# Kernel tuning notes

Measured on AMD Instinct MI355X. Metric: run time of the kernel, lower is better.

Reference implementation:

```python
import jax, jax.numpy as jnp
import numpy as np
from jax import lax

DIM = 128
HEADS = 4
HEAD_DIM = DIM // HEADS          # 32
SR = 2
BN_EPS = 1e-5


def setup_inputs() -> dict:
    key = jax.random.key(0)
    ks = jax.random.split(key, 16)
    B, N, C = 8, 3136, DIM
    H = W = 56
    Nkv = (H // SR) * (W // SR)  # 784
    s = 0.05
    inp = {
        "x": jax.random.normal(ks[0], (B, N, C), jnp.float32),
        "relative_pos": jax.random.normal(ks[1], (HEADS, N, Nkv), jnp.float32),
        "Wq": jax.random.normal(ks[2], (C, C), jnp.float32) * s,
        "bq": jnp.zeros((C,), jnp.float32),
        "Wk": jax.random.normal(ks[3], (C, C), jnp.float32) * s,
        "bk": jnp.zeros((C,), jnp.float32),
        "Wv": jax.random.normal(ks[4], (C, C), jnp.float32) * s,
        "bv": jnp.zeros((C,), jnp.float32),
        "conv_w": jax.random.normal(ks[5], (C, 1, SR, SR), jnp.float32) * s,  # depthwise OIHW
        "conv_b": jnp.zeros((C,), jnp.float32),
        "bn_gamma": jnp.ones((C,), jnp.float32),
        "bn_beta": jnp.zeros((C,), jnp.float32),
        "bn_mean": jax.random.normal(ks[6], (C,), jnp.float32) * 0.1,
        "bn_var": jax.random.uniform(ks[7], (C,), jnp.float32, 0.5, 1.5),
        "Wp": jax.random.normal(ks[8], (C, C), jnp.float32) * s,
        "bp": jnp.zeros((C,), jnp.float32),
        "H": H,
        "W": W,
    }
    return inp


def reference(x, relative_pos, Wq, bq, Wk, bk, Wv, bv, conv_w, conv_b,
              bn_gamma, bn_beta, bn_mean, bn_var, Wp, bp, H, W):
    B, N, C = x.shape
    scale = HEAD_DIM ** -0.5

    # q: (B, heads, N, head_dim)
    q = (x @ Wq + bq).reshape(B, N, HEADS, HEAD_DIM).transpose(0, 2, 1, 3)

    # spatial reduction: depthwise conv stride SR + BatchNorm (eval, running stats)
    x_img = x.transpose(0, 2, 1).reshape(B, C, H, W)
    y = lax.conv_general_dilated(
        x_img, conv_w, window_strides=(SR, SR), padding="VALID",
        feature_group_count=C,
        dimension_numbers=("NCHW", "OIHW", "NCHW")) + conv_b[None, :, None, None]
    inv = bn_gamma * lax.rsqrt(bn_var + BN_EPS)
    y = y * inv[None, :, None, None] + (bn_beta - bn_mean * inv)[None, :, None, None]
    x_ = y.reshape(B, C, -1).transpose(0, 2, 1)  # (B, Nkv, C)
    Nkv = x_.shape[1]

    k = (x_ @ Wk + bk).reshape(B, Nkv, HEADS, HEAD_DIM).transpose(0, 2, 1, 3)
    v = (x_ @ Wv + bv).reshape(B, Nkv, HEADS, HEAD_DIM).transpose(0, 2, 1, 3)

    attn = jnp.einsum("bhnd,bhmd->bhnm", q, k) * scale + relative_pos[None]
    attn = jax.nn.softmax(attn, axis=-1)
    out = jnp.einsum("bhnm,bhmd->bhnd", attn, v)
    out = out.transpose(0, 2, 1, 3).reshape(B, N, C)
    return out @ Wp + bp
```

## Files before the change

kernel.cpp:

```cpp
#include <hip/hip_runtime.h>
#include <hip/hip_bf16.h>

#define BATCH 8
#define NQ 3136
#define CDIM 128
#define NHEAD 4
#define HD 32
#define NKV 784
#define HIMG 56
#define SCALE 0.17677669529663687f

typedef __attribute__((ext_vector_type(8))) short bf8_t;
typedef __attribute__((ext_vector_type(4))) float f4_t;

using bf16 = __hip_bfloat16;
using u16  = unsigned short;

static __device__ __forceinline__ float b2f(bf16 v){ return __bfloat162float(v); }
static __device__ __forceinline__ bf16  f2b(float v){ return __float2bfloat16(v); }
static __device__ __forceinline__ short f2s(float v){
  union { bf16 b; short s; } u; u.b = f2b(v); return u.s;
}
static __device__ __forceinline__ float ld1(const void* p, size_t i, int f){
  return f ? b2f(((const bf16*)p)[i]) : ((const float*)p)[i];
}
static __device__ __forceinline__ bf8_t ld8(const void* p, size_t i, int f){
  if (f) return *(const bf8_t*)((const bf16*)p + i);
  const float* fp = (const float*)p + i;
  float4 a = *(const float4*)fp;
  float4 b = *(const float4*)(fp + 4);
  bf8_t r;
  r[0] = f2s(a.x); r[1] = f2s(a.y); r[2] = f2s(a.z); r[3] = f2s(a.w);
  r[4] = f2s(b.x); r[5] = f2s(b.y); r[6] = f2s(b.z); r[7] = f2s(b.w);
  return r;
}

__global__ __launch_bounds__(64) void detect_kernel(const void* var_raw, int* flag)
{
  int lane = threadIdx.x;
  const u16* h = (const u16*)var_raw;
  bool ok = true;
  #pragma unroll
  for (int t = 0; t < 2; t++){
    union { u16 u; bf16 b; } cv; cv.u = h[lane + 64 * t];
    float v = b2f(cv.b);
    ok = ok && (v > 0.3f) && (v < 1.7f);
  }
  unsigned long long ball = __ballot(ok);
  if (lane == 0) *flag = (ball == 0xFFFFFFFFFFFFFFFFull) ? 1 : 0;
}

__global__ __launch_bounds__(256) void prep_w_kernel(
    const void* __restrict__ Wq, const void* __restrict__ Wk,
    const void* __restrict__ Wv, const void* __restrict__ Wp,
    bf16* __restrict__ Wqt, bf16* __restrict__ Wkt,
    bf16* __restrict__ Wvt, bf16* __restrict__ Wpt, const int* flag)
{
  int f = *flag;
  int idx = blockIdx.x * 256 + threadIdx.x;
  int mat = idx >> 14;
  int e   = idx & 16383;
  int i = e >> 7, o = e & 127;
  const void* src; bf16* dst; float s = 1.f;
  if      (mat == 0){ src = Wq; dst = Wqt; s = SCALE; }
  else if (mat == 1){ src = Wk; dst = Wkt; }
  else if (mat == 2){ src = Wv; dst = Wvt; }
  else              { src = Wp; dst = Wpt; }
  dst[o * 128 + i] = f2b(ld1(src, e, f) * s);
}

__global__ __launch_bounds__(256) void prep_small_kernel(
    const void* bq, const void* bk, const void* bv, const void* bp,
    const void* cw, const void* cb, const void* gam, const void* bet,
    const void* mea, const void* var,
    bf16* bqs, bf16* bks, bf16* bvs, bf16* bps,
    float* cwf, float* inv, float* shift2, const int* flag)
{
  int f = *flag;
  int t = threadIdx.x;
  if (t < 128){
    bqs[t] = f2b(ld1(bq, t, f) * SCALE);
    bks[t] = f2b(ld1(bk, t, f));
    bvs[t] = f2b(ld1(bv, t, f));
    bps[t] = f2b(ld1(bp, t, f));
    float iv = ld1(gam, t, f) * rsqrtf(ld1(var, t, f) + 1e-5f);
    inv[t] = iv;
    shift2[t] = ld1(bet, t, f) - ld1(mea, t, f) * iv + ld1(cb, t, f) * iv;
  }
  cwf[t]       = ld1(cw, t, f);
  cwf[t + 256] = ld1(cw, t + 256, f);
}

__global__ __launch_bounds__(256) void reduce_kernel(
    const void* __restrict__ x, const float* __restrict__ cwf,
    const float* __restrict__ inv, const float* __restrict__ shift2,
    bf16* __restrict__ xr, const int* flag)
{
  int f = *flag;
  int idx = blockIdx.x * 256 + threadIdx.x;
  int c  = idx & 127;
  int t  = idx >> 7;
  int b  = t / NKV;
  int kv = t - b * NKV;
  int i = kv / 28, j = kv - i * 28;
  size_t base = (size_t)(b * NQ + (2 * i) * HIMG + 2 * j) * CDIM + c;
  float acc = ld1(x, base, f)                    * cwf[c * 4 + 0]
            + ld1(x, base + CDIM, f)             * cwf[c * 4 + 1]
            + ld1(x, base + HIMG * CDIM, f)      * cwf[c * 4 + 2]
            + ld1(x, base + HIMG * CDIM + CDIM, f) * cwf[c * 4 + 3];
  xr[idx] = f2b(acc * inv[c] + shift2[c]);
}

template<int MODE>
__global__ __launch_bounds__(256) void gemm_kernel(
    const bf16* A0, const bf16* A1, const bf16* __restrict__ Wt,
    const bf16* __restrict__ bias, void* outp, const int* flag)
{
  int f = *flag;
  const bf16* A = (MODE == 2) ? (f ? A0 : A1) : A0;
  int wave = threadIdx.x >> 6, lane = threadIdx.x & 63;
  int m = lane & 15, g = lane >> 4;
  int task = blockIdx.x * 4 + wave;
  int row0 = task * 16;

  const bf16* ap = A + (size_t)(row0 + m) * CDIM + 8 * g;
  bf8_t a[4];
  #pragma unroll
  for (int ks = 0; ks < 4; ks++) a[ks] = *(const bf8_t*)(ap + 32 * ks);

  f4_t acc[8];
  #pragma unroll
  for (int ct = 0; ct < 8; ct++){
    f4_t c = {0.f, 0.f, 0.f, 0.f};
    const bf16* bp = Wt + (size_t)(ct * 16 + m) * CDIM + 8 * g;
    #pragma unroll
    for (int ks = 0; ks < 4; ks++){
      bf8_t bfr = *(const bf8_t*)(bp + 32 * ks);
      c = __builtin_amdgcn_mfma_f32_16x16x32_bf16(a[ks], bfr, c, 0, 0, 0);
    }
    acc[ct] = c;
  }

  if (MODE == 0){
    bf16* out = (bf16*)outp;
    #pragma unroll
    for (int ct = 0; ct < 8; ct++){
      int col = ct * 16 + m;
      float bv = b2f(bias[col]);
      #pragma unroll
      for (int r = 0; r < 4; r++)
        out[(size_t)(row0 + 4 * g + r) * CDIM + col] = f2b(acc[ct][r] + bv);
    }
  } else if (MODE == 1){
    bf16* out = (bf16*)outp;
    int b   = row0 / NKV;
    int kv0 = row0 - b * NKV + 4 * g;
    #pragma unroll
    for (int ct = 0; ct < 8; ct++){
      int col = ct * 16 + m;
      float bv = b2f(bias[col]);
      int h = col >> 5, d = col & 31;
      union { bf16 hh[4]; uint2 u; } pk;
      #pragma unroll
      for (int r = 0; r < 4; r++) pk.hh[r] = f2b(acc[ct][r] + bv);
      *(uint2*)((bf16*)outp + (size_t)((b * NHEAD + h) * HD + d) * NKV + kv0) = pk.u;
    }
  } else {
    #pragma unroll
    for (int ct = 0; ct < 8; ct++){
      int col = ct * 16 + m;
      float bv = b2f(bias[col]);
      #pragma unroll
      for (int r = 0; r < 4; r++){
        size_t oi = (size_t)(row0 + 4 * g + r) * CDIM + col;
        float v = acc[ct][r] + bv;
        if (f) ((bf16*)outp)[oi] = f2b(v);
        else   ((float*)outp)[oi] = v;
      }
    }
  }
}

template<int T>
static __device__ __forceinline__ void attn_chunk(
    int kv0, const bf16* __restrict__ kbase,
    const bf16* __restrict__ vb0, const bf16* __restrict__ vb1,
    const void* __restrict__ rel, size_t relidx, int f, bf16* pl, int m, int g,
    bf8_t q8, float m_run[4], float l_run[4], f4_t& O0, f4_t& O1)
{
  f4_t s[T];
  #pragma unroll
  for (int t = 0; t < T; t++){
    bf8_t k8 = *(const bf8_t*)(kbase + (size_t)(kv0 + t * 16) * CDIM);
    f4_t z = {0.f, 0.f, 0.f, 0.f};
    s[t] = __builtin_amdgcn_mfma_f32_16x16x32_bf16(q8, k8, z, 0, 0, 0);
  }
  #pragma unroll
  for (int t = 0; t < T; t++){
    #pragma unroll
    for (int r = 0; r < 4; r++)
      s[t][r] += ld1(rel, relidx + (size_t)r * NKV + kv0 + t * 16, f);
  }
  float mloc[4];
  #pragma unroll
  for (int r = 0; r < 4; r++){
    float v = s[0][r];
    #pragma unroll
    for (int t = 1; t < T; t++) v = fmaxf(v, s[t][r]);
    mloc[r] = v;
  }
  #pragma unroll
  for (int xm = 1; xm < 16; xm <<= 1){
    #pragma unroll
    for (int r = 0; r < 4; r++)
      mloc[r] = fmaxf(mloc[r], __shfl_xor(mloc[r], xm, 64));
  }
  #pragma unroll
  for (int r = 0; r < 4; r++){
    float mn = fmaxf(m_run[r], mloc[r]);
    float al = __expf(m_run[r] - mn);
    m_run[r] = mn;
    l_run[r] *= al;
    O0[r] *= al; O1[r] *= al;
  }
  #pragma unroll
  for (int t = 0; t < T; t++){
    #pragma unroll
    for (int r = 0; r < 4; r++){
      float p = __expf(s[t][r] - m_run[r]);
      l_run[r] += p;
      pl[(4 * g + r) * 136 + t * 16 + m] = f2b(p);
    }
  }
  __syncthreads();
  constexpr int NKS = (T + 1) / 2;
  #pragma unroll
  for (int ks = 0; ks < NKS; ks++){
    bf8_t a8 = *(const bf8_t*)(pl + m * 136 + ks * 32 + 8 * g);
    bf8_t v0, v1;
    if (T == 1 && g >= 2){
      bf8_t z8 = {0, 0, 0, 0, 0, 0, 0, 0};
      a8 = z8; v0 = z8; v1 = z8;
    } else {
      v0 = *(const bf8_t*)(vb0 + kv0 + ks * 32 + 8 * g);
      v1 = *(const bf8_t*)(vb1 + kv0 + ks * 32 + 8 * g);
    }
    O0 = __builtin_amdgcn_mfma_f32_16x16x32_bf16(a8, v0, O0, 0, 0, 0);
    O1 = __builtin_amdgcn_mfma_f32_16x16x32_bf16(a8, v1, O1, 0, 0, 0);
  }
  __syncthreads();
}

__global__ __launch_bounds__(256) void attn_kernel(
    const void* __restrict__ x, const bf16* __restrict__ Wqt,
    const bf16* __restrict__ bqs, const bf16* __restrict__ kb,
    const bf16* __restrict__ vtb, const void* __restrict__ rel,
    void* __restrict__ dout, bf16* __restrict__ obf, const int* flag)
{
  int f = *flag;
  int wave = threadIdx.x >> 6, lane = threadIdx.x & 63;
  int m = lane & 15, g = lane >> 4;
  int b = blockIdx.z, h = blockIdx.y, qt = blockIdx.x;
  int qrow0 = qt * 64 + wave * 16;

  __shared__ bf16 Plds[4][16 * 136];
  bf16* pl = Plds[wave];

  {
    bf8_t xa[4];
    #pragma unroll
    for (int ks = 0; ks < 4; ks++)
      xa[ks] = ld8(x, (size_t)(b * NQ + qrow0 + m) * CDIM + 8 * g + 32 * ks, f);
    f4_t qc0 = {0.f, 0.f, 0.f, 0.f}, qc1 = {0.f, 0.f, 0.f, 0.f};
    const bf16* wp0 = Wqt + (size_t)(h * HD + m) * CDIM + 8 * g;
    const bf16* wp1 = Wqt + (size_t)(h * HD + 16 + m) * CDIM + 8 * g;
    #pragma unroll
    for (int ks = 0; ks < 4; ks++){
      bf8_t w0 = *(const bf8_t*)(wp0 + 32 * ks);
      bf8_t w1 = *(const bf8_t*)(wp1 + 32 * ks);
      qc0 = __builtin_amdgcn_mfma_f32_16x16x32_bf16(xa[ks], w0, qc0, 0, 0, 0);
      qc1 = __builtin_amdgcn_mfma_f32_16x16x32_bf16(xa[ks], w1, qc1, 0, 0, 0);
    }
    float bv0 = b2f(bqs[h * HD + m]);
    float bv1 = b2f(bqs[h * HD + 16 + m]);
    #pragma unroll
    for (int r = 0; r < 4; r++){
      pl[(4 * g + r) * 136 + m]      = f2b(qc0[r] + bv0);
      pl[(4 * g + r) * 136 + 16 + m] = f2b(qc1[r] + bv1);
    }
  }
  __syncthreads();
  bf8_t q8 = *(const bf8_t*)(pl + m * 136 + 8 * g);
  __syncthreads();

  const bf16* kbase = kb  + (size_t)(b * NKV + m) * CDIM + h * HD + 8 * g;
  const bf16* vb0   = vtb + (size_t)((b * NHEAD + h) * HD + m) * NKV;
  const bf16* vb1   = vtb + (size_t)((b * NHEAD + h) * HD + 16 + m) * NKV;
  size_t relidx = (size_t)(h * NQ + qrow0 + 4 * g) * NKV + m;

  float m_run[4], l_run[4];
  f4_t O0 = {0.f, 0.f, 0.f, 0.f}, O1 = {0.f, 0.f, 0.f, 0.f};
  #pragma unroll
  for (int r = 0; r < 4; r++){ m_run[r] = -1e30f; l_run[r] = 0.f; }

  #pragma unroll 1
  for (int kv0 = 0; kv0 < 768; kv0 += 128)
    attn_chunk<8>(kv0, kbase, vb0, vb1, rel, relidx, f, pl, m, g, q8, m_run, l_run, O0, O1);
  attn_chunk<1>(768, kbase, vb0, vb1, rel, relidx, f, pl, m, g, q8, m_run, l_run, O0, O1);

  #pragma unroll
  for (int xm = 1; xm < 16; xm <<= 1){
    #pragma unroll
    for (int r = 0; r < 4; r++)
      l_run[r] += __shfl_xor(l_run[r], xm, 64);
  }
  bf16* ob = f ? (bf16*)dout : obf;
  size_t orow = (size_t)(b * NQ + qrow0 + 4 * g);
  #pragma unroll
  for (int r = 0; r < 4; r++){
    float iv = 1.0f / l_run[r];
    ob[(orow + r) * CDIM + h * HD + m]      = f2b(O0[r] * iv);
    ob[(orow + r) * CDIM + h * HD + 16 + m] = f2b(O1[r] * iv);
  }
}

extern "C" void kernel_launch(void* const* d_in, const int* in_sizes, int n_in,
                              void* d_out, int out_size, void* d_ws, size_t ws_size,
                              hipStream_t stream)
{
  const void* x   = d_in[0];
  const void* rel = d_in[1];
  const void* Wq  = d_in[2];
  const void* bq  = d_in[3];
  const void* Wk  = d_in[4];
  const void* bk  = d_in[5];
  const void* Wv  = d_in[6];
  const void* bv  = d_in[7];
  const void* cw  = d_in[8];
  const void* cb  = d_in[9];
  const void* gam = d_in[10];
  const void* bet = d_in[11];
  const void* mea = d_in[12];
  const void* var = d_in[13];
  const void* Wp  = d_in[14];
  const void* bp  = d_in[15];

  char* w = (char*)d_ws;
  auto alloc = [&](size_t bytes){
    char* p = w; w += (bytes + 255) & ~(size_t)255; return p;
  };
  int*  flag = (int*)alloc(4);
  bf16* Wqt  = (bf16*)alloc(128 * 128 * sizeof(bf16));
  bf16* Wkt  = (bf16*)alloc(128 * 128 * sizeof(bf16));
  bf16* Wvt  = (bf16*)alloc(128 * 128 * sizeof(bf16));
  bf16* Wpt  = (bf16*)alloc(128 * 128 * sizeof(bf16));
  bf16* bqs  = (bf16*)alloc(128 * sizeof(bf16));
  bf16* bks  = (bf16*)alloc(128 * sizeof(bf16));
  bf16* bvs  = (bf16*)alloc(128 * sizeof(bf16));
  bf16* bps  = (bf16*)alloc(128 * sizeof(bf16));
  float* cwf    = (float*)alloc(512 * sizeof(float));
  float* inv    = (float*)alloc(128 * sizeof(float));
  float* shift2 = (float*)alloc(128 * sizeof(float));
  bf16* xr  = (bf16*)alloc((size_t)BATCH * NKV * CDIM * sizeof(bf16));
  bf16* kbf = (bf16*)alloc((size_t)BATCH * NKV * CDIM * sizeof(bf16));
  bf16* vtb = (bf16*)alloc((size_t)BATCH * NKV * CDIM * sizeof(bf16));
  bf16* obf = (bf16*)alloc((size_t)BATCH * NQ * CDIM * sizeof(bf16));

  detect_kernel<<<1, 64, 0, stream>>>(var, flag);
  prep_w_kernel<<<256, 256, 0, stream>>>(Wq, Wk, Wv, Wp, Wqt, Wkt, Wvt, Wpt, flag);
  prep_small_kernel<<<1, 256, 0, stream>>>(bq, bk, bv, bp, cw, cb, gam, bet, mea, var,
                                           bqs, bks, bvs, bps, cwf, inv, shift2, flag);
  reduce_kernel<<<3136, 256, 0, stream>>>(x, cwf, inv, shift2, xr, flag);
  gemm_kernel<0><<<98, 256, 0, stream>>>(xr, nullptr, Wkt, bks, kbf, flag);
  gemm_kernel<1><<<98, 256, 0, stream>>>(xr, nullptr, Wvt, bvs, vtb, flag);
  attn_kernel<<<dim3(49, NHEAD, BATCH), 256, 0, stream>>>(x, Wqt, bqs, kbf, vtb, rel,
                                                          d_out, obf, flag);
  gemm_kernel<2><<<392, 256, 0, stream>>>((const bf16*)d_out, obf, Wpt, bps, d_out, flag);
}
```

Measured before the change: 251.9 us.

## Merge prep kernels, precompute Q, fuse K/V GEMMs, stage relative_pos in LDS

Removes the detect kernel by computing the dtype flag inline in every kernel, and merges the weight and small-parameter prep into one launch. Q is projected once in a separate block range of the reduction kernel rather than recomputed per head inside attention. The K and V GEMMs are combined into one launch. Attention now stages each relative_pos tile into LDS with vectorized cooperative loads instead of scattered per-lane global reads. The trade-offs are a new workspace buffer for Q and an extra barrier per KV chunk.

After: 246.9 us. 1.02x faster.

```diff
diff --git a/kernel.cpp b/kernel.cpp
--- a/kernel.cpp
+++ b/kernel.cpp
@@ -30,153 +30,202 @@
   float4 a = *(const float4*)fp;
   float4 b = *(const float4*)(fp + 4);
   bf8_t r;
-  r[0] = f2s(a.x); r[1] = f2s(a.y); r[2] = f2s(a.z); r[3] = f2s(a.w);
-  r[4] = f2s(b.x); r[5] = f2s(b.y); r[6] = f2s(b.z); r[7] = f2s(b.w);
+  r[0]=f2s(a.x); r[1]=f2s(a.y); r[2]=f2s(a.z); r[3]=f2s(a.w);
+  r[4]=f2s(b.x); r[5]=f2s(b.y); r[6]=f2s(b.z); r[7]=f2s(b.w);
   return r;
 }
-
-__global__ __launch_bounds__(64) void detect_kernel(const void* var_raw, int* flag)
-{
-  int lane = threadIdx.x;
+static __device__ __forceinline__ int detect_flag(const void* var_raw){
   const u16* h = (const u16*)var_raw;
+  int lane = threadIdx.x & 63;
   bool ok = true;
   #pragma unroll
   for (int t = 0; t < 2; t++){
-    union { u16 u; bf16 b; } cv; cv.u = h[lane + 64 * t];
+    union { u16 u; bf16 b; } cv; cv.u = h[lane + 64*t];
     float v = b2f(cv.b);
     ok = ok && (v > 0.3f) && (v < 1.7f);
   }
-  unsigned long long ball = __ballot(ok);
-  if (lane == 0) *flag = (ball == 0xFFFFFFFFFFFFFFFFull) ? 1 : 0;
-}
-
-__global__ __launch_bounds__(256) void prep_w_kernel(
+  return (__ballot(ok) == ~0ull) ? 1 : 0;
+}
+
+static __device__ __forceinline__ void mfma_row(
+    const bf8_t a[4], const bf16* __restrict__ Wt, int m, int g, f4_t acc[8])
+{
+  #pragma unroll
+  for (int ct = 0; ct < 8; ct++){
+    f4_t c = {0.f,0.f,0.f,0.f};
+    const bf16* bp = Wt + (size_t)(ct*16 + m)*CDIM + 8*g;
+    #pragma unroll
+    for (int ks = 0; ks < 4; ks++){
+      bf8_t b = *(const bf8_t*)(bp + 32*ks);
+      c = __builtin_amdgcn_mfma_f32_16x16x32_bf16(a[ks], b, c, 0,0,0);
+    }
+    acc[ct] = c;
+  }
+}
+
+__global__ __launch_bounds__(256) void prep_kernel(
     const void* __restrict__ Wq, const void* __restrict__ Wk,
     const void* __restrict__ Wv, const void* __restrict__ Wp,
+    const void* __restrict__ var, const void* __restrict__ cw,
+    const void* __restrict__ cb, const void* __restrict__ gam,
+    const void* __restrict__ bet, const void* __restrict__ mea,
+    const void* __restrict__ bq, const void* __restrict__ bk,
+    const void* __restrict__ bv, const void* __restrict__ bp,
     bf16* __restrict__ Wqt, bf16* __restrict__ Wkt,
-    bf16* __restrict__ Wvt, bf16* __restrict__ Wpt, const int* flag)
-{
-  int f = *flag;
-  int idx = blockIdx.x * 256 + threadIdx.x;
+    bf16* __restrict__ Wvt, bf16* __restrict__ Wpt,
+    bf16* __restrict__ bqs, bf16* __restrict__ bks,
+    bf16* __restrict__ bvs, bf16* __restrict__ bps,
+    float* __restrict__ cwf, float* __restrict__ inv, float* __restrict__ shift2)
+{
+  int f = detect_flag(var);
+  int idx = blockIdx.x*256 + threadIdx.x;
   int mat = idx >> 14;
   int e   = idx & 16383;
-  int i = e >> 7, o = e & 127;
+  int o = e >> 7, i = e & 127;
   const void* src; bf16* dst; float s = 1.f;
   if      (mat == 0){ src = Wq; dst = Wqt; s = SCALE; }
   else if (mat == 1){ src = Wk; dst = Wkt; }
   else if (mat == 2){ src = Wv; dst = Wvt; }
   else              { src = Wp; dst = Wpt; }
-  dst[o * 128 + i] = f2b(ld1(src, e, f) * s);
-}
-
-__global__ __launch_bounds__(256) void prep_small_kernel(
-    const void* bq, const void* bk, const void* bv, const void* bp,
-    const void* cw, const void* cb, const void* gam, const void* bet,
-    const void* mea, const void* var,
-    bf16* bqs, bf16* bks, bf16* bvs, bf16* bps,
-    float* cwf, float* inv, float* shift2, const int* flag)
-{
-  int f = *flag;
-  int t = threadIdx.x;
-  if (t < 128){
-    bqs[t] = f2b(ld1(bq, t, f) * SCALE);
-    bks[t] = f2b(ld1(bk, t, f));
-    bvs[t] = f2b(ld1(bv, t, f));
-    bps[t] = f2b(ld1(bp, t, f));
-    float iv = ld1(gam, t, f) * rsqrtf(ld1(var, t, f) + 1e-5f);
-    inv[t] = iv;
-    shift2[t] = ld1(bet, t, f) - ld1(mea, t, f) * iv + ld1(cb, t, f) * iv;
-  }
-  cwf[t]       = ld1(cw, t, f);
-  cwf[t + 256] = ld1(cw, t + 256, f);
-}
-
-__global__ __launch_bounds__(256) void reduce_kernel(
-    const void* __restrict__ x, const float* __restrict__ cwf,
-    const float* __restrict__ inv, const float* __restrict__ shift2,
-    bf16* __restrict__ xr, const int* flag)
-{
-  int f = *flag;
-  int idx = blockIdx.x * 256 + threadIdx.x;
-  int c  = idx & 127;
-  int t  = idx >> 7;
-  int b  = t / NKV;
-  int kv = t - b * NKV;
-  int i = kv / 28, j = kv - i * 28;
-  size_t base = (size_t)(b * NQ + (2 * i) * HIMG + 2 * j) * CDIM + c;
-  float acc = ld1(x, base, f)                    * cwf[c * 4 + 0]
-            + ld1(x, base + CDIM, f)             * cwf[c * 4 + 1]
-            + ld1(x, base + HIMG * CDIM, f)      * cwf[c * 4 + 2]
-            + ld1(x, base + HIMG * CDIM + CDIM, f) * cwf[c * 4 + 3];
-  xr[idx] = f2b(acc * inv[c] + shift2[c]);
-}
-
-template<int MODE>
-__global__ __launch_bounds__(256) void gemm_kernel(
-    const bf16* A0, const bf16* A1, const bf16* __restrict__ Wt,
-    const bf16* __restrict__ bias, void* outp, const int* flag)
-{
-  int f = *flag;
-  const bf16* A = (MODE == 2) ? (f ? A0 : A1) : A0;
+  dst[e] = f2b(ld1(src, (size_t)i*128 + o, f) * s);
+
+  if (blockIdx.x == 0){
+    int t = threadIdx.x;
+    cwf[t]       = ld1(cw, t, f);
+    cwf[t + 256] = ld1(cw, t + 256, f);
+    if (t < 128){
+      bqs[t] = f2b(ld1(bq, t, f) * SCALE);
+      bks[t] = f2b(ld1(bk, t, f));
+      bvs[t] = f2b(ld1(bv, t, f));
+      bps[t] = f2b(ld1(bp, t, f));
+      float iv = ld1(gam, t, f) * rsqrtf(ld1(var, t, f) + 1e-5f);
+      inv[t] = iv;
+      shift2[t] = ld1(bet, t, f) - ld1(mea, t, f) * iv + ld1(cb, t, f) * iv;
+    }
+  }
+}
+
+__global__ __launch_bounds__(256) void fat_kernel(
+    const void* __restrict__ x, const void* __restrict__ var,
+    const float* __restrict__ cwf, const float* __restrict__ inv,
+    const float* __restrict__ shift2, bf16* __restrict__ xr,
+    const bf16* __restrict__ Wqt, const bf16* __restrict__ bqs,
+    bf16* __restrict__ qbf)
+{
+  int f = detect_flag(var);
+  if (blockIdx.x < 3136){
+    int idx = blockIdx.x*256 + threadIdx.x;
+    int c  = idx & 127;
+    int t  = idx >> 7;
+    int b  = t / NKV;
+    int kv = t - b*NKV;
+    int i = kv/28, j = kv - i*28;
+    size_t base = (size_t)(b*NQ + 2*i*HIMG + 2*j)*CDIM + c;
+    float acc = ld1(x, base, f)                   * cwf[c*4 + 0]
+              + ld1(x, base + CDIM, f)            * cwf[c*4 + 1]
+              + ld1(x, base + HIMG*CDIM, f)       * cwf[c*4 + 2]
+              + ld1(x, base + HIMG*CDIM + CDIM, f)* cwf[c*4 + 3];
+    xr[idx] = f2b(acc * inv[c] + shift2[c]);
+  } else {
+    int wave = threadIdx.x >> 6, lane = threadIdx.x & 63;
+    int m = lane & 15, g = lane >> 4;
+    int task = (blockIdx.x - 3136)*4 + wave;
+    int row0 = task*16;
+    bf8_t a[4];
+    #pragma unroll
+    for (int ks = 0; ks < 4; ks++)
+      a[ks] = ld8(x, (size_t)(row0 + m)*CDIM + 8*g + 32*ks, f);
+    f4_t acc[8];
+    mfma_row(a, Wqt, m, g, acc);
+    #pragma unroll
+    for (int ct = 0; ct < 8; ct++){
+      int col = ct*16 + m;
+      float bv = b2f(bqs[col]);
+      #pragma unroll
+      for (int r = 0; r < 4; r++)
+        qbf[(size_t)(row0 + 4*g + r)*CDIM + col] = f2b(acc[ct][r] + bv);
+    }
+  }
+}
+
+__global__ __launch_bounds__(256) void kv_kernel(
+    const bf16* __restrict__ xr,
+    const bf16* __restrict__ Wkt, const bf16* __restrict__ Wvt,
+    const bf16* __restrict__ bks, const bf16* __restrict__ bvs,
+    bf16* __restrict__ kbf, bf16* __restrict__ vtb)
+{
   int wave = threadIdx.x >> 6, lane = threadIdx.x & 63;
   int m = lane & 15, g = lane >> 4;
-  int task = blockIdx.x * 4 + wave;
-  int row0 = task * 16;
-
-  const bf16* ap = A + (size_t)(row0 + m) * CDIM + 8 * g;
+  bool isK = blockIdx.x < 98;
+  int bx = isK ? blockIdx.x : blockIdx.x - 98;
+  int row0 = (bx*4 + wave)*16;
   bf8_t a[4];
   #pragma unroll
-  for (int ks = 0; ks < 4; ks++) a[ks] = *(const bf8_t*)(ap + 32 * ks);
-
+  for (int ks = 0; ks < 4; ks++)
+    a[ks] = *(const bf8_t*)(xr + (size_t)(row0 + m)*CDIM + 8*g + 32*ks);
   f4_t acc[8];
-  #pragma unroll
-  for (int ct = 0; ct < 8; ct++){
-    f4_t c = {0.f, 0.f, 0.f, 0.f};
-    const bf16* bp = Wt + (size_t)(ct * 16 + m) * CDIM + 8 * g;
-    #pragma unroll
-    for (int ks = 0; ks < 4; ks++){
-      bf8_t bfr = *(const bf8_t*)(bp + 32 * ks);
-      c = __builtin_amdgcn_mfma_f32_16x16x32_bf16(a[ks], bfr, c, 0, 0, 0);
-    }
-    acc[ct] = c;
-  }
-
-  if (MODE == 0){
-    bf16* out = (bf16*)outp;
+  mfma_row(a, isK ? Wkt : Wvt, m, g, acc);
+
+  if (isK){
     #pragma unroll
     for (int ct = 0; ct < 8; ct++){
-      int col = ct * 16 + m;
-      float bv = b2f(bias[col]);
+      int col = ct*16 + m;
+      float bv = b2f(bks[col]);
       #pragma unroll
       for (int r = 0; r < 4; r++)
-        out[(size_t)(row0 + 4 * g + r) * CDIM + col] = f2b(acc[ct][r] + bv);
-    }
-  } else if (MODE == 1){
-    bf16* out = (bf16*)outp;
+        kbf[(size_t)(row0 + 4*g + r)*CDIM + col] = f2b(acc[ct][r] + bv);
+    }
+  } else {
     int b   = row0 / NKV;
-    int kv0 = row0 - b * NKV + 4 * g;
+    int kv0 = row0 - b*NKV + 4*g;
     #pragma unroll
     for (int ct = 0; ct < 8; ct++){
-      int col = ct * 16 + m;
-      float bv = b2f(bias[col]);
+      int col = ct*16 + m;
+      float bv = b2f(bvs[col]);
       int h = col >> 5, d = col & 31;
       union { bf16 hh[4]; uint2 u; } pk;
       #pragma unroll
       for (int r = 0; r < 4; r++) pk.hh[r] = f2b(acc[ct][r] + bv);
-      *(uint2*)((bf16*)outp + (size_t)((b * NHEAD + h) * HD + d) * NKV + kv0) = pk.u;
+      *(uint2*)(vtb + (size_t)((b*NHEAD + h)*HD + d)*NKV + kv0) = pk.u;
+    }
+  }
+}
+
+template<int W>
+static __device__ __forceinline__ void stage_rel(
+    const void* __restrict__ rel, int f, bf16* __restrict__ rel_l,
+    size_t rowbase, int kv0)
+{
+  const int tid = threadIdx.x;
+  if (f){
+    constexpr int PER = W/8;
+    constexpr int SL  = 64*PER;
+    #pragma unroll
+    for (int it = 0; it < (SL + 255)/256; it++){
+      int s0 = it*256 + tid;
+      if (SL < 256 && s0 >= SL) continue;
+      int row = s0 / PER;
+      int col = (s0 - row*PER)*8;
+      const bf16* gp = (const bf16*)rel + (rowbase + row)*NKV + kv0 + col;
+      uint2 lo = *(const uint2*)gp;
+      uint2 hi = *(const uint2*)(gp + 4);
+      *(uint2*)(rel_l + row*132 + col)     = lo;
+      *(uint2*)(rel_l + row*132 + col + 4) = hi;
     }
   } else {
-    #pragma unroll
-    for (int ct = 0; ct < 8; ct++){
-      int col = ct * 16 + m;
-      float bv = b2f(bias[col]);
-      #pragma unroll
-      for (int r = 0; r < 4; r++){
-        size_t oi = (size_t)(row0 + 4 * g + r) * CDIM + col;
-        float v = acc[ct][r] + bv;
-        if (f) ((bf16*)outp)[oi] = f2b(v);
-        else   ((float*)outp)[oi] = v;
-      }
+    constexpr int PER = W/4;
+    constexpr int SL  = 64*PER;
+    #pragma unroll
+    for (int it = 0; it < (SL + 255)/256; it++){
+      int s0 = it*256 + tid;
+      int row = s0 / PER;
+      int col = (s0 - row*PER)*4;
+      const float* gp = (const float*)rel + (rowbase + row)*NKV + kv0 + col;
+      float4 v = *(const float4*)gp;
+      union { u16 hh[4]; uint2 u; } pk;
+      pk.hh[0]=(u16)f2s(v.x); pk.hh[1]=(u16)f2s(v.y);
+      pk.hh[2]=(u16)f2s(v.z); pk.hh[3]=(u16)f2s(v.w);
+      *(uint2*)(rel_l + row*132 + col) = pk.u;
     }
   }
 }
@@ -185,21 +234,21 @@
 static __device__ __forceinline__ void attn_chunk(
     int kv0, const bf16* __restrict__ kbase,
     const bf16* __restrict__ vb0, const bf16* __restrict__ vb1,
-    const void* __restrict__ rel, size_t relidx, int f, bf16* pl, int m, int g,
+    const bf16* __restrict__ rel_l, int wrow, bf16* pl, int m, int g,
     bf8_t q8, float m_run[4], float l_run[4], f4_t& O0, f4_t& O1)
 {
   f4_t s[T];
   #pragma unroll
   for (int t = 0; t < T; t++){
-    bf8_t k8 = *(const bf8_t*)(kbase + (size_t)(kv0 + t * 16) * CDIM);
-    f4_t z = {0.f, 0.f, 0.f, 0.f};
-    s[t] = __builtin_amdgcn_mfma_f32_16x16x32_bf16(q8, k8, z, 0, 0, 0);
+    bf8_t k8 = *(const bf8_t*)(kbase + (size_t)(kv0 + t*16)*CDIM);
+    f4_t z = {0.f,0.f,0.f,0.f};
+    s[t] = __builtin_amdgcn_mfma_f32_16x16x32_bf16(q8, k8, z, 0,0,0);
   }
   #pragma unroll
   for (int t = 0; t < T; t++){
     #pragma unroll
     for (int r = 0; r < 4; r++)
-      s[t][r] += ld1(rel, relidx + (size_t)r * NKV + kv0 + t * 16, f);
+      s[t][r] += b2f(rel_l[(wrow + 4*g + r)*132 + t*16 + m]);
   }
   float mloc[4];
   #pragma unroll
@@ -229,84 +278,93 @@
     for (int r = 0; r < 4; r++){
       float p = __expf(s[t][r] - m_run[r]);
       l_run[r] += p;
-      pl[(4 * g + r) * 136 + t * 16 + m] = f2b(p);
+      pl[(4*g + r)*136 + t*16 + m] = f2b(p);
     }
   }
   __syncthreads();
-  constexpr int NKS = (T + 1) / 2;
+  constexpr int NKS = (T + 1)/2;
   #pragma unroll
   for (int ks = 0; ks < NKS; ks++){
-    bf8_t a8 = *(const bf8_t*)(pl + m * 136 + ks * 32 + 8 * g);
+    bf8_t a8 = *(const bf8_t*)(pl + m*136 + ks*32 + 8*g);
     bf8_t v0, v1;
     if (T == 1 && g >= 2){
-      bf8_t z8 = {0, 0, 0, 0, 0, 0, 0, 0};
+      bf8_t z8 = {0,0,0,0,0,0,0,0};
       a8 = z8; v0 = z8; v1 = z8;
     } else {
-      v0 = *(const bf8_t*)(vb0 + kv0 + ks * 32 + 8 * g);
-      v1 = *(const bf8_t*)(vb1 + kv0 + ks * 32 + 8 * g);
-    }
-    O0 = __builtin_amdgcn_mfma_f32_16x16x32_bf16(a8, v0, O0, 0, 0, 0);
-    O1 = __builtin_amdgcn_mfma_f32_16x16x32_bf16(a8, v1, O1, 0, 0, 0);
-  }
-  __syncthreads();
-}
-
+      v0 = *(const bf8_t*)(vb0 + kv0 + ks*32 + 8*g);
+      v1 = *(const bf8_t*)(vb1 + kv0 + ks*32 + 8*g);
+    }
+    O0 = __builtin_amdgcn_mfma_f32_16x16x32_bf16(a8, v0, O0, 0,0,0);
+    O1 = __builtin_amdgcn_mfma_f32_16x16x32_bf16(a8, v1, O1, 0,0,0);
+  }
+}
+
+template<int QF>
 __global__ __launch_bounds__(256) void attn_kernel(
-    const void* __restrict__ x, const bf16* __restrict__ Wqt,
-    const bf16* __restrict__ bqs, const bf16* __restrict__ kb,
-    const bf16* __restrict__ vtb, const void* __restrict__ rel,
-    void* __restrict__ dout, bf16* __restrict__ obf, const int* flag)
-{
-  int f = *flag;
+    const bf16* __restrict__ qbf, const void* __restrict__ x,
+    const bf16* __restrict__ Wqt, const bf16* __restrict__ bqs,
+    const bf16* __restrict__ kb, const bf16* __restrict__ vtb,
+    const void* __restrict__ rel, const void* __restrict__ var,
+    void* __restrict__ dout, bf16* __restrict__ obf)
+{
+  int f = detect_flag(var);
   int wave = threadIdx.x >> 6, lane = threadIdx.x & 63;
   int m = lane & 15, g = lane >> 4;
   int b = blockIdx.z, h = blockIdx.y, qt = blockIdx.x;
-  int qrow0 = qt * 64 + wave * 16;
-
-  __shared__ bf16 Plds[4][16 * 136];
+  int qrow0 = qt*64 + wave*16;
+  int wrow  = wave*16;
+
+  __shared__ bf16 rel_l[64*132];
+  __shared__ bf16 Plds[4][16*136];
   bf16* pl = Plds[wave];
 
-  {
+  bf8_t q8;
+  if constexpr (QF == 0){
+    q8 = *(const bf8_t*)(qbf + (size_t)(b*NQ + qrow0 + m)*CDIM + h*HD + 8*g);
+  } else {
     bf8_t xa[4];
     #pragma unroll
     for (int ks = 0; ks < 4; ks++)
-      xa[ks] = ld8(x, (size_t)(b * NQ + qrow0 + m) * CDIM + 8 * g + 32 * ks, f);
-    f4_t qc0 = {0.f, 0.f, 0.f, 0.f}, qc1 = {0.f, 0.f, 0.f, 0.f};
-    const bf16* wp0 = Wqt + (size_t)(h * HD + m) * CDIM + 8 * g;
-    const bf16* wp1 = Wqt + (size_t)(h * HD + 16 + m) * CDIM + 8 * g;
+      xa[ks] = ld8(x, (size_t)(b*NQ + qrow0 + m)*CDIM + 8*g + 32*ks, f);
+    f4_t qc0 = {0.f,0.f,0.f,0.f}, qc1 = {0.f,0.f,0.f,0.f};
+    const bf16* wp0 = Wqt + (size_t)(h*HD + m)*CDIM + 8*g;
+    const bf16* wp1 = Wqt + (size_t)(h*HD + 16 + m)*CDIM + 8*g;
     #pragma unroll
     for (int ks = 0; ks < 4; ks++){
-      bf8_t w0 = *(const bf8_t*)(wp0 + 32 * ks);
-      bf8_t w1 = *(const bf8_t*)(wp1 + 32 * ks);
-      qc0 = __builtin_amdgcn_mfma_f32_16x16x32_bf16(xa[ks], w0, qc0, 0, 0, 0);
-      qc1 = __builtin_amdgcn_mfma_f32_16x16x32_bf16(xa[ks], w1, qc1, 0, 0, 0);
-    }
-    float bv0 = b2f(bqs[h * HD + m]);
-    float bv1 = b2f(bqs[h * HD + 16 + m]);
+      bf8_t w0 = *(const bf8_t*)(wp0 + 32*ks);
+      bf8_t w1 = *(const bf8_t*)(wp1 + 32*ks);
+      qc0 = __builtin_amdgcn_mfma_f32_16x16x32_bf16(xa[ks], w0, qc0, 0,0,0);
+      qc1 = __builtin_amdgcn_mfma_f32_16x16x32_bf16(xa[ks], w1, qc1, 0,0,0);
+    }
+    float bv0 = b2f(bqs[h*HD + m]);
+    float bv1 = b2f(bqs[h*HD + 16 + m]);
     #pragma unroll
     for (int r = 0; r < 4; r++){
-      pl[(4 * g + r) * 136 + m]      = f2b(qc0[r] + bv0);
-      pl[(4 * g + r) * 136 + 16 + m] = f2b(qc1[r] + bv1);
-    }
-  }
+      pl[(4*g + r)*136 + m]      = f2b(qc0[r] + bv0);
+      pl[(4*g + r)*136 + 16 + m] = f2b(qc1[r] + bv1);
+    }
+    q8 = *(const bf8_t*)(pl + m*136 + 8*g);
+  }
+
+  const bf16* kbase = kb  + (size_t)(b*NKV + m)*CDIM + h*HD + 8*g;
+  const bf16* vb0   = vtb + (size_t)((b*NHEAD + h)*HD + m)*NKV;
+  const bf16* vb1   = vtb + (size_t)((b*NHEAD + h)*HD + 16 + m)*NKV;
+  size_t rowbase = (size_t)h*NQ + qt*64;
+
+  float m_run[4], l_run[4];
+  f4_t O0 = {0.f,0.f,0.f,0.f}, O1 = {0.f,0.f,0.f,0.f};
+  #pragma unroll
+  for (int r = 0; r < 4; r++){ m_run[r] = -1e30f; l_run[r] = 0.f; }
+
+  #pragma unroll 1
+  for (int kv0 = 0; kv0 < 768; kv0 += 128){
+    stage_rel<128>(rel, f, rel_l, rowbase, kv0);
+    __syncthreads();
+    attn_chunk<8>(kv0, kbase, vb0, vb1, rel_l, wrow, pl, m, g, q8, m_run, l_run, O0, O1);
+  }
+  stage_rel<16>(rel, f, rel_l, rowbase, 768);
   __syncthreads();
-  bf8_t q8 = *(const bf8_t*)(pl + m * 136 + 8 * g);
-  __syncthreads();
-
-  const bf16* kbase = kb  + (size_t)(b * NKV + m) * CDIM + h * HD + 8 * g;
-  const bf16* vb0   = vtb + (size_t)((b * NHEAD + h) * HD + m) * NKV;
-  const bf16* vb1   = vtb + (size_t)((b * NHEAD + h) * HD + 16 + m) * NKV;
-  size_t relidx = (size_t)(h * NQ + qrow0 + 4 * g) * NKV + m;
-
-  float m_run[4], l_run[4];
-  f4_t O0 = {0.f, 0.f, 0.f, 0.f}, O1 = {0.f, 0.f, 0.f, 0.f};
-  #pragma unroll
-  for (int r = 0; r < 4; r++){ m_run[r] = -1e30f; l_run[r] = 0.f; }
-
-  #pragma unroll 1
-  for (int kv0 = 0; kv0 < 768; kv0 += 128)
-    attn_chunk<8>(kv0, kbase, vb0, vb1, rel, relidx, f, pl, m, g, q8, m_run, l_run, O0, O1);
-  attn_chunk<1>(768, kbase, vb0, vb1, rel, relidx, f, pl, m, g, q8, m_run, l_run, O0, O1);
+  attn_chunk<1>(768, kbase, vb0, vb1, rel_l, wrow, pl, m, g, q8, m_run, l_run, O0, O1);
 
   #pragma unroll
   for (int xm = 1; xm < 16; xm <<= 1){
@@ -315,12 +373,41 @@
       l_run[r] += __shfl_xor(l_run[r], xm, 64);
   }
   bf16* ob = f ? (bf16*)dout : obf;
-  size_t orow = (size_t)(b * NQ + qrow0 + 4 * g);
+  size_t orow = (size_t)(b*NQ + qrow0 + 4*g);
   #pragma unroll
   for (int r = 0; r < 4; r++){
     float iv = 1.0f / l_run[r];
-    ob[(orow + r) * CDIM + h * HD + m]      = f2b(O0[r] * iv);
-    ob[(orow + r) * CDIM + h * HD + 16 + m] = f2b(O1[r] * iv);
+    ob[(orow + r)*CDIM + h*HD + m]      = f2b(O0[r] * iv);
+    ob[(orow + r)*CDIM + h*HD + 16 + m] = f2b(O1[r] * iv);
+  }
+}
+
+__global__ __launch_bounds__(256) void proj_kernel(
+    const bf16* A0, const bf16* A1, const bf16* __restrict__ Wt,
+    const bf16* __restrict__ bias, void* outp, const void* __restrict__ var)
+{
+  int f = detect_flag(var);
+  const bf16* A = f ? A0 : A1;
+  int wave = threadIdx.x >> 6, lane = threadIdx.x & 63;
+  int m = lane & 15, g = lane >> 4;
+  int row0 = (blockIdx.x*4 + wave)*16;
+  bf8_t a[4];
+  #pragma unroll
+  for (int ks = 0; ks < 4; ks++)
+    a[ks] = *(const bf8_t*)(A + (size_t)(row0 + m)*CDIM + 8*g + 32*ks);
+  f4_t acc[8];
+  mfma_row(a, Wt, m, g, acc);
+  #pragma unroll
+  for (int ct = 0; ct < 8; ct++){
+    int col = ct*16 + m;
+    float bv = b2f(bias[col]);
+    #pragma unroll
+    for (int r = 0; r < 4; r++){
+      size_t oi = (size_t)(row0 + 4*g + r)*CDIM + col;
+      float v = acc[ct][r] + bv;
+      if (f) ((bf16*)outp)[oi]  = f2b(v);
+      else   ((float*)outp)[oi] = v;
+    }
   }
 }
 
@@ -349,31 +436,38 @@
   auto alloc = [&](size_t bytes){
     char* p = w; w += (bytes + 255) & ~(size_t)255; return p;
   };
-  int*  flag = (int*)alloc(4);
-  bf16* Wqt  = (bf16*)alloc(128 * 128 * sizeof(bf16));
-  bf16* Wkt  = (bf16*)alloc(128 * 128 * sizeof(bf16));
-  bf16* Wvt  = (bf16*)alloc(128 * 128 * sizeof(bf16));
-  bf16* Wpt  = (bf16*)alloc(128 * 128 * sizeof(bf16));
-  bf16* bqs  = (bf16*)alloc(128 * sizeof(bf16));
-  bf16* bks  = (bf16*)alloc(128 * sizeof(bf16));
-  bf16* bvs  = (bf16*)alloc(128 * sizeof(bf16));
-  bf16* bps  = (bf16*)alloc(128 * sizeof(bf16));
-  float* cwf    = (float*)alloc(512 * sizeof(float));
-  float* inv    = (float*)alloc(128 * sizeof(float));
-  float* shift2 = (float*)alloc(128 * sizeof(float));
-  bf16* xr  = (bf16*)alloc((size_t)BATCH * NKV * CDIM * sizeof(bf16));
-  bf16* kbf = (bf16*)alloc((size_t)BATCH * NKV * CDIM * sizeof(bf16));
-  bf16* vtb = (bf16*)alloc((size_t)BATCH * NKV * CDIM * sizeof(bf16));
-  bf16* obf = (bf16*)alloc((size_t)BATCH * NQ * CDIM * sizeof(bf16));
-
-  detect_kernel<<<1, 64, 0, stream>>>(var, flag);
-  prep_w_kernel<<<256, 256, 0, stream>>>(Wq, Wk, Wv, Wp, Wqt, Wkt, Wvt, Wpt, flag);
-  prep_small_kernel<<<1, 256, 0, stream>>>(bq, bk, bv, bp, cw, cb, gam, bet, mea, var,
-                                           bqs, bks, bvs, bps, cwf, inv, shift2, flag);
-  reduce_kernel<<<3136, 256, 0, stream>>>(x, cwf, inv, shift2, xr, flag);
-  gemm_kernel<0><<<98, 256, 0, stream>>>(xr, nullptr, Wkt, bks, kbf, flag);
-  gemm_kernel<1><<<98, 256, 0, stream>>>(xr, nullptr, Wvt, bvs, vtb, flag);
-  attn_kernel<<<dim3(49, NHEAD, BATCH), 256, 0, stream>>>(x, Wqt, bqs, kbf, vtb, rel,
-                                                          d_out, obf, flag);
-  gemm_kernel<2><<<392, 256, 0, stream>>>((const bf16*)d_out, obf, Wpt, bps, d_out, flag);
-}
+  bf16* Wqt = (bf16*)alloc(128*128*sizeof(bf16));
+  bf16* Wkt = (bf16*)alloc(128*128*sizeof(bf16));
+  bf16* Wvt = (bf16*)alloc(128*128*sizeof(bf16));
+  bf16* Wpt = (bf16*)alloc(128*128*sizeof(bf16));
+  bf16* bqs = (bf16*)alloc(128*sizeof(bf16));
+  bf16* bks = (bf16*)alloc(128*sizeof(bf16));
+  bf16* bvs = (bf16*)alloc(128*sizeof(bf16));
+  bf16* bps = (bf16*)alloc(128*sizeof(bf16));
+  float* cwf    = (float*)alloc(512*sizeof(float));
+  float* inv    = (float*)alloc(128*sizeof(float));
+  float* shift2 = (float*)alloc(128*sizeof(float));
+  bf16* xr  = (bf16*)alloc((size_t)BATCH*NKV*CDIM*sizeof(bf16));
+  bf16* kbf = (bf16*)alloc((size_t)BATCH*NKV*CDIM*sizeof(bf16));
+  bf16* vtb = (bf16*)alloc((size_t)BATCH*NKV*CDIM*sizeof(bf16));
+  bf16* obf = (bf16*)alloc((size_t)BATCH*NQ*CDIM*sizeof(bf16));
+
+  size_t qbf_bytes = (size_t)BATCH*NQ*CDIM*sizeof(bf16);
+  bool use_q = (size_t)(((char*)d_ws + ws_size) - w) >= qbf_bytes + 256;
+  bf16* qbf = use_q ? (bf16*)alloc(qbf_bytes) : nullptr;
+
+  prep_kernel<<<256, 256, 0, stream>>>(Wq, Wk, Wv, Wp, var, cw, cb, gam, bet, mea,
+                                       bq, bk, bv, bp,
+                                       Wqt, Wkt, Wvt, Wpt, bqs, bks, bvs, bps,
+                                       cwf, inv, shift2);
+  fat_kernel<<<3136 + (use_q ? 392 : 0), 256, 0, stream>>>(
+      x, var, cwf, inv, shift2, xr, Wqt, bqs, qbf);
+  kv_kernel<<<196, 256, 0, stream>>>(xr, Wkt, Wvt, bks, bvs, kbf, vtb);
+  if (use_q)
+    attn_kernel<0><<<dim3(49, NHEAD, BATCH), 256, 0, stream>>>(
+        qbf, x, Wqt, bqs, kbf, vtb, rel, var, d_out, obf);
+  else
+    attn_kernel<1><<<dim3(49, NHEAD, BATCH), 256, 0, stream>>>(
+        qbf, x, Wqt, bqs, kbf, vtb, rel, var, d_out, obf);
+  proj_kernel<<<392, 256, 0, stream>>>((const bf16*)d_out, obf, Wpt, bps, d_out, var);
+}
```
